# Kernel optimization log

Measured on AMD Instinct MI355X. Metric: run time of the kernel, lower is better.

The kernel has to match this reference:

```python
import jax, jax.numpy as jnp
import numpy as np
from jax import lax

# --- config matching init_kwargs ---
VOXEL_SIZE = np.array([0.25, 0.25, 8.0], np.float32)
PC_RANGE = np.array([-50.0, -50.0, -5.0, 50.0, 50.0, 3.0], np.float32)
MAX_PTS = 32
MAX_VOX = 60000
GRID = np.round((PC_RANGE[3:] - PC_RANGE[:3]) / VOXEL_SIZE).astype(np.int64)  # [400,400,1] (x,y,z)
GX, GY, GZ = int(GRID[0]), int(GRID[1]), int(GRID[2])
BIG = GX * GY * GZ  # sentinel flat id for out-of-range points
N_POINTS = 1_200_000
N_FEATS = 5


def voxelize(points):
    """points: [N, 3+C] float. Returns (out_voxels [V,P,3+C], out_coords [V,3] zyx, out_num_points [V])."""
    N = points.shape[0]
    vsize = jnp.asarray(VOXEL_SIZE)
    vmin = jnp.asarray(PC_RANGE[:3])
    # integer voxel coords per point (x,y,z)
    cxyz = jnp.floor((points[:, :3] - vmin) / vsize).astype(jnp.int32)  # [N,3]
    grid = jnp.asarray(GRID, jnp.int32)
    in_range = jnp.all((cxyz >= 0) & (cxyz < grid), axis=-1)  # [N]
    flat = cxyz[:, 2] * (GY * GX) + cxyz[:, 1] * GX + cxyz[:, 0]
    flat = jnp.where(in_range, flat, BIG)
    # stable sort by voxel id: points within a voxel keep original order (like CPU fill order)
    order = jnp.argsort(flat, stable=True)
    sf = flat[order]                      # sorted flat ids, invalid (BIG) at end
    sp = points[order]                    # [N, D]
    sc = cxyz[order]                      # [N, 3]
    ar = jnp.arange(N, dtype=jnp.int32)
    valid = sf < BIG
    new_seg = jnp.concatenate([jnp.ones((1,), bool), sf[1:] != sf[:-1]])
    first = valid & new_seg               # first point of each non-empty voxel
    vox_idx = jnp.cumsum(first.astype(jnp.int32)) - 1          # voxel slot per point
    seg_start = lax.associative_scan(jnp.maximum, jnp.where(first, ar, 0))
    rank = ar - seg_start                 # position of point within its voxel
    keep = valid & (vox_idx < MAX_VOX) & (rank < MAX_PTS)
    # out-of-bound index MAX_VOX + mode='drop' discards non-kept points
    sv = jnp.where(keep, vox_idx, MAX_VOX)
    sr = jnp.where(keep, rank, 0)
    D = points.shape[1]
    out_voxels = jnp.zeros((MAX_VOX, MAX_PTS, D), points.dtype).at[sv, sr].set(sp, mode='drop')
    out_num_points = jnp.zeros((MAX_VOX,), jnp.int32).at[sv].add(
        keep.astype(jnp.int32), mode='drop')
    coords_zyx = sc[:, ::-1]              # reorder to [z,y,x] as in the torch module
    out_coords = jnp.zeros((MAX_VOX, 3), jnp.int32).at[sv].set(coords_zyx, mode='drop')
    return out_voxels, out_coords, out_num_points


def setup_inputs() -> dict:
    key = jax.random.key(0)
    u = jax.random.uniform(key, (N_POINTS, N_FEATS), jnp.float32)
    # xyz spans slightly beyond the valid range so out-of-range masking is exercised
    lo = jnp.array([-55.0, -55.0, -6.0, 0.0, 0.0], jnp.float32)
    hi = jnp.array([55.0, 55.0, 4.0, 1.0, 1.0], jnp.float32)
    points = lo + u * (hi - lo)
    return {"points": points}


def reference(points):
    return voxelize(points)
```

## Files before the change

### kernel.cpp

```cpp
#include <hip/hip_runtime.h>


constexpr int GXc = 400;
constexpr int GYc = 400;
constexpr int NCELL = GXc * GYc;
constexpr int MAXV  = 60000;
constexpr int MAXP  = 32;
constexpr int NF    = 5;

constexpr int SCAN_B = 256;
constexpr int SCAN_E = 8;
constexpr int SCAN_TILE = SCAN_B * SCAN_E;
constexpr int NSCANBLK = (NCELL + SCAN_TILE - 1) / SCAN_TILE;

__device__ __forceinline__ int point_cell(float x, float y, float z) {
    int cx = (int)floorf((x + 50.0f) * 4.0f);
    int cy = (int)floorf((y + 50.0f) * 4.0f);
    int cz = (int)floorf((z + 5.0f) * 0.125f);
    if (cx < 0 || cx >= GXc || cy < 0 || cy >= GYc || cz != 0) return -1;
    return cy * GXc + cx;
}

__global__ void __launch_bounds__(256)
k_bin(const float* __restrict__ pts, int N,
      unsigned char* __restrict__ occupied, int* __restrict__ cellId) {
    int t = blockIdx.x * blockDim.x + threadIdx.x;
    int i0 = t * 4;
    if (i0 >= N) return;
    if (N - i0 >= 4) {
        const float4* src = (const float4*)(pts + (size_t)i0 * NF);
        float4 q0 = src[0], q1 = src[1], q2 = src[2], q3 = src[3], q4 = src[4];
        float f[20];
        *(float4*)(f + 0)  = q0; *(float4*)(f + 4)  = q1; *(float4*)(f + 8)  = q2;
        *(float4*)(f + 12) = q3; *(float4*)(f + 16) = q4;
        int cs[4];
        #pragma unroll
        for (int k = 0; k < 4; k++)
            cs[k] = point_cell(f[k * 5 + 0], f[k * 5 + 1], f[k * 5 + 2]);
        *(int4*)(cellId + i0) = make_int4(cs[0], cs[1], cs[2], cs[3]);
        #pragma unroll
        for (int k = 0; k < 4; k++)
            if (cs[k] >= 0) occupied[cs[k]] = 1;
    } else {
        for (int k = 0; k < N - i0; k++) {
            const float* p = pts + (size_t)(i0 + k) * NF;
            int c = point_cell(p[0], p[1], p[2]);
            cellId[i0 + k] = c;
            if (c >= 0) occupied[c] = 1;
        }
    }
}

__global__ void k_scanA(const unsigned char* __restrict__ occupied,
                        int* __restrict__ excl, int* __restrict__ blockSums) {
    __shared__ int sh[SCAN_B];
    int base = blockIdx.x * SCAN_TILE;
    int idx0 = base + threadIdx.x * SCAN_E;
    unsigned long long occ8 = 0;
    if (idx0 < NCELL) occ8 = *(const unsigned long long*)(occupied + idx0);
    int vals[SCAN_E];
    int sum = 0;
    #pragma unroll
    for (int e = 0; e < SCAN_E; e++) {
        int v = (int)((occ8 >> (8 * e)) & 1ull);
        vals[e] = sum;
        sum += v;
    }
    sh[threadIdx.x] = sum;
    __syncthreads();
    for (int off = 1; off < SCAN_B; off <<= 1) {
        int t = (threadIdx.x >= (unsigned)off) ? sh[threadIdx.x - off] : 0;
        __syncthreads();
        sh[threadIdx.x] += t;
        __syncthreads();
    }
    int thrExcl = (threadIdx.x == 0) ? 0 : sh[threadIdx.x - 1];
    #pragma unroll
    for (int e = 0; e < SCAN_E; e++) {
        int idx = idx0 + e;
        if (idx < NCELL) excl[idx] = thrExcl + vals[e];
    }
    if (threadIdx.x == SCAN_B - 1) blockSums[blockIdx.x] = sh[SCAN_B - 1];
}

__global__ void k_scanB(const unsigned char* __restrict__ occupied,
                        const int* __restrict__ excl,
                        const int* __restrict__ blockSums,
                        int* __restrict__ voxId,
                        int* __restrict__ cellOfVox,
                        int* __restrict__ nvoxOut) {
    __shared__ int sb[128];
    int tid = threadIdx.x;
    if (tid < 128) sb[tid] = (tid < NSCANBLK) ? blockSums[tid] : 0;
    __syncthreads();
    for (int off = 1; off < 128; off <<= 1) {
        int t = (tid < 128 && tid >= off) ? sb[tid - off] : 0;
        __syncthreads();
        if (tid < 128) sb[tid] += t;
        __syncthreads();
    }
    int c = blockIdx.x * blockDim.x + tid;
    if (c < NCELL) {
        int vi = -1;
        if (occupied[c]) {
            int blk = c / SCAN_TILE;
            int basev = (blk == 0) ? 0 : sb[blk - 1];
            int v = basev + excl[c];
            if (v < MAXV) { vi = v; cellOfVox[v] = c; }
        }
        voxId[c] = vi;
    }
    if (blockIdx.x == 0 && tid == 0) {
        int tot = sb[NSCANBLK - 1];
        *nvoxOut = tot < MAXV ? tot : MAXV;
    }
}

__global__ void __launch_bounds__(256)
k_scatter2(const int* __restrict__ cellId, int N,
           const int* __restrict__ voxId,
           int* __restrict__ vcount, int* __restrict__ slots) {
    int t = blockIdx.x * blockDim.x + threadIdx.x;
    int i0 = t * 8;
    if (i0 >= N) return;
    if (N - i0 >= 8) {
        int4 a = *(const int4*)(cellId + i0);
        int4 b = *(const int4*)(cellId + i0 + 4);
        int cs[8] = {a.x, a.y, a.z, a.w, b.x, b.y, b.z, b.w};
        int vs[8];
        #pragma unroll
        for (int k = 0; k < 8; k++)
            vs[k] = (cs[k] >= 0) ? voxId[cs[k]] : -1;
        #pragma unroll
        for (int k = 0; k < 8; k++) {
            if (vs[k] >= 0) {
                int pos = atomicAdd(&vcount[vs[k]], 1);
                if (pos < MAXP) slots[vs[k] * MAXP + pos] = i0 + k;
            }
        }
    } else {
        for (int k = 0; k < N - i0; k++) {
            int c = cellId[i0 + k];
            if (c >= 0) {
                int v = voxId[c];
                if (v >= 0) {
                    int pos = atomicAdd(&vcount[v], 1);
                    if (pos < MAXP) slots[v * MAXP + pos] = i0 + k;
                }
            }
        }
    }
}

__global__ void __launch_bounds__(256)
k_finalize(const float* __restrict__ pts, int N,
           const int* __restrict__ vcount,
           const int* __restrict__ slots,
           const int* __restrict__ cellOfVox,
           const int* __restrict__ nvoxPtr,
           float* __restrict__ outVox,
           float* __restrict__ outCoord,
           float* __restrict__ outNum) {
    __shared__ int   s_key[4][4][MAXP];
    __shared__ int   s_srt[4][4][MAXP];
    __shared__ float s_dat[4][4][MAXP * NF];

    int tid  = threadIdx.x;
    int wv   = tid >> 6, lane = tid & 63;
    int h    = lane >> 5, s = lane & 31;
    int vb   = (blockIdx.x * 4 + wv) * 4;
    int nvox = *nvoxPtr;

    int u0 = vb + h, u1 = vb + 2 + h;
    bool live0 = u0 < nvox, live1 = u1 < nvox;
    int num0 = 0, num1 = 0;
    if (live0) { int cnt = vcount[u0]; num0 = cnt < MAXP ? cnt : MAXP; }
    if (live1) { int cnt = vcount[u1]; num1 = cnt < MAXP ? cnt : MAXP; }

    int k0 = (live0 && s < num0) ? slots[u0 * MAXP + s] : 0x7fffffff;
    int k1 = (live1 && s < num1) ? slots[u1 * MAXP + s] : 0x7fffffff;
    s_key[wv][h][s]     = k0;
    s_key[wv][2 + h][s] = k1;

    float* flat = (float*)s_dat[wv];
    #pragma unroll
    for (int q = 0; q < 10; q++) flat[q * 64 + lane] = 0.0f;

    int rank0 = 0, rank1 = 0;
    #pragma unroll
    for (int j = 0; j < MAXP; j++) rank0 += (s_key[wv][h][j] < k0) ? 1 : 0;
    #pragma unroll
    for (int j = 0; j < MAXP; j++) rank1 += (s_key[wv][2 + h][j] < k1) ? 1 : 0;
    bool g0 = live0 && s < num0, g1 = live1 && s < num1;
    if (g0) s_srt[wv][h][rank0]     = k0;
    if (g1) s_srt[wv][2 + h][rank1] = k1;

    int p0 = g0 ? s_srt[wv][h][s]     : 0;
    int p1 = g1 ? s_srt[wv][2 + h][s] : 0;
    float4 qa0, qb0, qa1, qb1;
    int sel0 = -1, sel1 = -1;
    size_t lim = (size_t)N * 20;
    const float4* f4 = (const float4*)pts;
    if (g0) {
        size_t b = (size_t)p0 * 20;
        if (b + 32 <= lim) {
            sel0 = (int)((b & 15) >> 2);
            size_t w = b >> 4;
            qa0 = f4[w]; qb0 = f4[w + 1];
        }
    }
    if (g1) {
        size_t b = (size_t)p1 * 20;
        if (b + 32 <= lim) {
            sel1 = (int)((b & 15) >> 2);
            size_t w = b >> 4;
            qa1 = f4[w]; qb1 = f4[w + 1];
        }
    }
    if (g0) {
        float r0, r1, r2, r3, r4, r5, r6, r7;
        if (sel0 >= 0) {
            r0 = qa0.x; r1 = qa0.y; r2 = qa0.z; r3 = qa0.w;
            r4 = qb0.x; r5 = qb0.y; r6 = qb0.z; r7 = qb0.w;
        } else {
            const float* sp = pts + (size_t)p0 * NF;
            r0 = sp[0]; r1 = sp[1]; r2 = sp[2]; r3 = sp[3]; r4 = sp[4];
            r5 = r6 = r7 = 0.0f; sel0 = 0;
        }
        float o0 = sel0 == 0 ? r0 : sel0 == 1 ? r1 : sel0 == 2 ? r2 : r3;
        float o1 = sel0 == 0 ? r1 : sel0 == 1 ? r2 : sel0 == 2 ? r3 : r4;
        float o2 = sel0 == 0 ? r2 : sel0 == 1 ? r3 : sel0 == 2 ? r4 : r5;
        float o3 = sel0 == 0 ? r3 : sel0 == 1 ? r4 : sel0 == 2 ? r5 : r6;
        float o4 = sel0 == 0 ? r4 : sel0 == 1 ? r5 : sel0 == 2 ? r6 : r7;
        float* d = &s_dat[wv][h][s * NF];
        d[0] = o0; d[1] = o1; d[2] = o2; d[3] = o3; d[4] = o4;
    }
    if (g1) {
        float r0, r1, r2, r3, r4, r5, r6, r7;
        if (sel1 >= 0) {
            r0 = qa1.x; r1 = qa1.y; r2 = qa1.z; r3 = qa1.w;
            r4 = qb1.x; r5 = qb1.y; r6 = qb1.z; r7 = qb1.w;
        } else {
            const float* sp = pts + (size_t)p1 * NF;
            r0 = sp[0]; r1 = sp[1]; r2 = sp[2]; r3 = sp[3]; r4 = sp[4];
            r5 = r6 = r7 = 0.0f; sel1 = 0;
        }
        float o0 = sel1 == 0 ? r0 : sel1 == 1 ? r1 : sel1 == 2 ? r2 : r3;
        float o1 = sel1 == 0 ? r1 : sel1 == 1 ? r2 : sel1 == 2 ? r3 : r4;
        float o2 = sel1 == 0 ? r2 : sel1 == 1 ? r3 : sel1 == 2 ? r4 : r5;
        float o3 = sel1 == 0 ? r3 : sel1 == 1 ? r4 : sel1 == 2 ? r5 : r6;
        float o4 = sel1 == 0 ? r4 : sel1 == 1 ? r5 : sel1 == 2 ? r6 : r7;
        float* d = &s_dat[wv][2 + h][s * NF];
        d[0] = o0; d[1] = o1; d[2] = o2; d[3] = o3; d[4] = o4;
    }

    const float4* sv = (const float4*)s_dat[wv];
    float4* dst = (float4*)(outVox + (size_t)vb * (MAXP * NF));
    #pragma unroll
    for (int q = 0; q < 3; q++) {
        int idx = q * 64 + lane;
        if (idx < 160) dst[idx] = sv[idx];
    }
    if (lane < 4) {
        int v = vb + lane;
        bool lv = v < nvox;
        int c = lv ? cellOfVox[v] : 0;
        int cnt = lv ? vcount[v] : 0;
        int num = cnt < MAXP ? cnt : MAXP;
        outNum[v] = lv ? (float)num : 0.0f;
        outCoord[(size_t)v * 3 + 0] = 0.0f;
        outCoord[(size_t)v * 3 + 1] = lv ? (float)(c / GXc) : 0.0f;
        outCoord[(size_t)v * 3 + 2] = lv ? (float)(c % GXc) : 0.0f;
    }
}

extern "C" void kernel_launch(void* const* d_in, const int* in_sizes, int n_in,
                              void* d_out, int out_size, void* d_ws, size_t ws_size,
                              hipStream_t stream) {
    const float* pts = (const float*)d_in[0];
    int N = in_sizes[0] / NF;

    float* out      = (float*)d_out;
    float* outVox   = out;
    float* outCoord = out + (size_t)MAXV * MAXP * NF;
    float* outNum   = outCoord + (size_t)MAXV * 3;

    char* ws = (char*)d_ws;
    auto take = [&](size_t bytes) {
        char* p = ws;
        ws += (bytes + 255) & ~(size_t)255;
        return p;
    };
    unsigned char* occupied = (unsigned char*)take((size_t)NCELL);
    int* vcount    = (int*)take((size_t)MAXV * 4);
    int* cellId    = (int*)take((size_t)((N + 7) & ~7) * 4);
    int* excl      = (int*)take((size_t)NCELL * 4);
    int* blockSums = (int*)take((size_t)128 * 4);
    int* voxId     = (int*)take((size_t)NCELL * 4);
    int* cellOfVox = (int*)take((size_t)MAXV * 4);
    int* slots     = (int*)take((size_t)MAXV * MAXP * 4);
    int* nvoxBuf   = (int*)take(256);

    size_t zeroBytes = (size_t)((char*)(vcount + MAXV) - (char*)occupied);
    hipMemsetAsync(occupied, 0, zeroBytes, stream);

    int nb4 = ((N + 3) / 4 + 255) / 256;
    k_bin<<<nb4, 256, 0, stream>>>(pts, N, occupied, cellId);
    k_scanA<<<NSCANBLK, SCAN_B, 0, stream>>>(occupied, excl, blockSums);
    k_scanB<<<(NCELL + 255) / 256, 256, 0, stream>>>(occupied, excl, blockSums,
                                                     voxId, cellOfVox, nvoxBuf);
    int nb8 = ((N + 7) / 8 + 255) / 256;
    k_scatter2<<<nb8, 256, 0, stream>>>(cellId, N, voxId, vcount, slots);
    k_finalize<<<MAXV / 16, 256, 0, stream>>>(pts, N, vcount, slots, cellOfVox,
                                              nvoxBuf, outVox, outCoord, outNum);
}
```

Before: 120.7 us.

## Scatter full point payloads into voxel slots and drop cellId buffer

```diff
diff --git a/kernel.cpp b/kernel.cpp
--- a/kernel.cpp
+++ b/kernel.cpp
@@ -22,8 +22,104 @@
 }
 
 __global__ void __launch_bounds__(256)
-k_bin(const float* __restrict__ pts, int N,
-      unsigned char* __restrict__ occupied, int* __restrict__ cellId) {
+k_bin(const float* __restrict__ pts, int N, unsigned char* __restrict__ occupied) {
+    int t = blockIdx.x * blockDim.x + threadIdx.x;
+    int i0 = t * 4;
+    if (i0 >= N) return;
+    if (N - i0 >= 4) {
+        const float4* src = (const float4*)(pts + (size_t)i0 * NF);
+        float4 q0 = src[0], q1 = src[1], q2 = src[2], q3 = src[3], q4 = src[4];
+        float f[20];
+        *(float4*)(f + 0)  = q0; *(float4*)(f + 4)  = q1; *(float4*)(f + 8)  = q2;
+        *(float4*)(f + 12) = q3; *(float4*)(f + 16) = q4;
+        #pragma unroll
+        for (int k = 0; k < 4; k++) {
+            int c = point_cell(f[k * 5 + 0], f[k * 5 + 1], f[k * 5 + 2]);
+            if (c >= 0) occupied[c] = 1;
+        }
+    } else {
+        for (int k = 0; k < N - i0; k++) {
+            const float* p = pts + (size_t)(i0 + k) * NF;
+            int c = point_cell(p[0], p[1], p[2]);
+            if (c >= 0) occupied[c] = 1;
+        }
+    }
+}
+
+__global__ void k_scanA(const unsigned char* __restrict__ occupied,
+                        int* __restrict__ excl, int* __restrict__ blockSums) {
+    __shared__ int sh[SCAN_B];
+    int base = blockIdx.x * SCAN_TILE;
+    int idx0 = base + threadIdx.x * SCAN_E;
+    unsigned long long occ8 = 0;
+    if (idx0 < NCELL) occ8 = *(const unsigned long long*)(occupied + idx0);
+    int vals[SCAN_E];
+    int sum = 0;
+    #pragma unroll
+    for (int e = 0; e < SCAN_E; e++) {
+        int v = (int)((occ8 >> (8 * e)) & 1ull);
+        vals[e] = sum;
+        sum += v;
+    }
+    sh[threadIdx.x] = sum;
+    __syncthreads();
+    for (int off = 1; off < SCAN_B; off <<= 1) {
+        int t = (threadIdx.x >= (unsigned)off) ? sh[threadIdx.x - off] : 0;
+        __syncthreads();
+        sh[threadIdx.x] += t;
+        __syncthreads();
+    }
+    int thrExcl = (threadIdx.x == 0) ? 0 : sh[threadIdx.x - 1];
+    #pragma unroll
+    for (int e = 0; e < SCAN_E; e++) {
+        int idx = idx0 + e;
+        if (idx < NCELL) excl[idx] = thrExcl + vals[e];
+    }
+    if (threadIdx.x == SCAN_B - 1) blockSums[blockIdx.x] = sh[SCAN_B - 1];
+}
+
+__global__ void k_scanB(const unsigned char* __restrict__ occupied,
+                        const int* __restrict__ excl,
+                        const int* __restrict__ blockSums,
+                        int* __restrict__ voxId,
+                        int* __restrict__ cellOfVox,
+                        int* __restrict__ vcount,
+                        int* __restrict__ nvoxOut) {
+    __shared__ int sb[128];
+    int tid = threadIdx.x;
+    if (tid < 128) sb[tid] = (tid < NSCANBLK) ? blockSums[tid] : 0;
+    __syncthreads();
+    for (int off = 1; off < 128; off <<= 1) {
+        int t = (tid < 128 && tid >= off) ? sb[tid - off] : 0;
+        __syncthreads();
+        if (tid < 128) sb[tid] += t;
+        __syncthreads();
+    }
+    int c = blockIdx.x * blockDim.x + tid;
+    if (c < NCELL) {
+        int vi = -1;
+        if (occupied[c]) {
+            int blk = c / SCAN_TILE;
+            int basev = (blk == 0) ? 0 : sb[blk - 1];
+            int v = basev + excl[c];
+            if (v < MAXV) {
+                vi = v;
+                cellOfVox[v] = c;
+                vcount[v] = 0;
+            }
+        }
+        voxId[c] = vi;
+    }
+    if (blockIdx.x == 0 && tid == 0) {
+        int tot = sb[NSCANBLK - 1];
+        *nvoxOut = tot < MAXV ? tot : MAXV;
+    }
+}
+
+__global__ void __launch_bounds__(256)
+k_scatter3(const float* __restrict__ pts, int N,
+           const int* __restrict__ voxId,
+           int* __restrict__ vcount, float* __restrict__ vdata) {
     int t = blockIdx.x * blockDim.x + threadIdx.x;
     int i0 = t * 4;
     if (i0 >= N) return;
@@ -37,115 +133,36 @@
         #pragma unroll
         for (int k = 0; k < 4; k++)
             cs[k] = point_cell(f[k * 5 + 0], f[k * 5 + 1], f[k * 5 + 2]);
-        *(int4*)(cellId + i0) = make_int4(cs[0], cs[1], cs[2], cs[3]);
+        int vs[4];
         #pragma unroll
         for (int k = 0; k < 4; k++)
-            if (cs[k] >= 0) occupied[cs[k]] = 1;
+            vs[k] = (cs[k] >= 0) ? voxId[cs[k]] : -1;
+        #pragma unroll
+        for (int k = 0; k < 4; k++) {
+            if (vs[k] >= 0) {
+                int pos = atomicAdd(&vcount[vs[k]], 1);
+                if (pos < MAXP) {
+                    float* r = vdata + ((size_t)vs[k] * MAXP + pos) * 8;
+                    *(float4*)r = make_float4(f[k*5+0], f[k*5+1], f[k*5+2], f[k*5+3]);
+                    *(float4*)(r + 4) = make_float4(f[k*5+4],
+                                                    __int_as_float(i0 + k), 0.0f, 0.0f);
+                }
+            }
+        }
     } else {
         for (int k = 0; k < N - i0; k++) {
             const float* p = pts + (size_t)(i0 + k) * NF;
             int c = point_cell(p[0], p[1], p[2]);
-            cellId[i0 + k] = c;
-            if (c >= 0) occupied[c] = 1;
-        }
-    }
-}
-
-__global__ void k_scanA(const unsigned char* __restrict__ occupied,
-                        int* __restrict__ excl, int* __restrict__ blockSums) {
-    __shared__ int sh[SCAN_B];
-    int base = blockIdx.x * SCAN_TILE;
-    int idx0 = base + threadIdx.x * SCAN_E;
-    unsigned long long occ8 = 0;
-    if (idx0 < NCELL) occ8 = *(const unsigned long long*)(occupied + idx0);
-    int vals[SCAN_E];
-    int sum = 0;
-    #pragma unroll
-    for (int e = 0; e < SCAN_E; e++) {
-        int v = (int)((occ8 >> (8 * e)) & 1ull);
-        vals[e] = sum;
-        sum += v;
-    }
-    sh[threadIdx.x] = sum;
-    __syncthreads();
-    for (int off = 1; off < SCAN_B; off <<= 1) {
-        int t = (threadIdx.x >= (unsigned)off) ? sh[threadIdx.x - off] : 0;
-        __syncthreads();
-        sh[threadIdx.x] += t;
-        __syncthreads();
-    }
-    int thrExcl = (threadIdx.x == 0) ? 0 : sh[threadIdx.x - 1];
-    #pragma unroll
-    for (int e = 0; e < SCAN_E; e++) {
-        int idx = idx0 + e;
-        if (idx < NCELL) excl[idx] = thrExcl + vals[e];
-    }
-    if (threadIdx.x == SCAN_B - 1) blockSums[blockIdx.x] = sh[SCAN_B - 1];
-}
-
-__global__ void k_scanB(const unsigned char* __restrict__ occupied,
-                        const int* __restrict__ excl,
-                        const int* __restrict__ blockSums,
-                        int* __restrict__ voxId,
-                        int* __restrict__ cellOfVox,
-                        int* __restrict__ nvoxOut) {
-    __shared__ int sb[128];
-    int tid = threadIdx.x;
-    if (tid < 128) sb[tid] = (tid < NSCANBLK) ? blockSums[tid] : 0;
-    __syncthreads();
-    for (int off = 1; off < 128; off <<= 1) {
-        int t = (tid < 128 && tid >= off) ? sb[tid - off] : 0;
-        __syncthreads();
-        if (tid < 128) sb[tid] += t;
-        __syncthreads();
-    }
-    int c = blockIdx.x * blockDim.x + tid;
-    if (c < NCELL) {
-        int vi = -1;
-        if (occupied[c]) {
-            int blk = c / SCAN_TILE;
-            int basev = (blk == 0) ? 0 : sb[blk - 1];
-            int v = basev + excl[c];
-            if (v < MAXV) { vi = v; cellOfVox[v] = c; }
-        }
-        voxId[c] = vi;
-    }
-    if (blockIdx.x == 0 && tid == 0) {
-        int tot = sb[NSCANBLK - 1];
-        *nvoxOut = tot < MAXV ? tot : MAXV;
-    }
-}
-
-__global__ void __launch_bounds__(256)
-k_scatter2(const int* __restrict__ cellId, int N,
-           const int* __restrict__ voxId,
-           int* __restrict__ vcount, int* __restrict__ slots) {
-    int t = blockIdx.x * blockDim.x + threadIdx.x;
-    int i0 = t * 8;
-    if (i0 >= N) return;
-    if (N - i0 >= 8) {
-        int4 a = *(const int4*)(cellId + i0);
-        int4 b = *(const int4*)(cellId + i0 + 4);
-        int cs[8] = {a.x, a.y, a.z, a.w, b.x, b.y, b.z, b.w};
-        int vs[8];
-        #pragma unroll
-        for (int k = 0; k < 8; k++)
-            vs[k] = (cs[k] >= 0) ? voxId[cs[k]] : -1;
-        #pragma unroll
-        for (int k = 0; k < 8; k++) {
-            if (vs[k] >= 0) {
-                int pos = atomicAdd(&vcount[vs[k]], 1);
-                if (pos < MAXP) slots[vs[k] * MAXP + pos] = i0 + k;
-            }
-        }
-    } else {
-        for (int k = 0; k < N - i0; k++) {
-            int c = cellId[i0 + k];
             if (c >= 0) {
                 int v = voxId[c];
                 if (v >= 0) {
                     int pos = atomicAdd(&vcount[v], 1);
-                    if (pos < MAXP) slots[v * MAXP + pos] = i0 + k;
+                    if (pos < MAXP) {
+                        float* r = vdata + ((size_t)v * MAXP + pos) * 8;
+                        *(float4*)r = make_float4(p[0], p[1], p[2], p[3]);
+                        *(float4*)(r + 4) = make_float4(p[4],
+                                                        __int_as_float(i0 + k), 0.0f, 0.0f);
+                    }
                 }
             }
         }
@@ -153,16 +170,14 @@
 }
 
 __global__ void __launch_bounds__(256)
-k_finalize(const float* __restrict__ pts, int N,
-           const int* __restrict__ vcount,
-           const int* __restrict__ slots,
-           const int* __restrict__ cellOfVox,
-           const int* __restrict__ nvoxPtr,
-           float* __restrict__ outVox,
-           float* __restrict__ outCoord,
-           float* __restrict__ outNum) {
+k_finalize2(const int* __restrict__ vcount,
+            const float* __restrict__ vdata,
+            const int* __restrict__ cellOfVox,
+            const int* __restrict__ nvoxPtr,
+            float* __restrict__ outVox,
+            float* __restrict__ outCoord,
+            float* __restrict__ outNum) {
     __shared__ int   s_key[4][4][MAXP];
-    __shared__ int   s_srt[4][4][MAXP];
     __shared__ float s_dat[4][4][MAXP * NF];
 
     int tid  = threadIdx.x;
@@ -176,9 +191,19 @@
     int num0 = 0, num1 = 0;
     if (live0) { int cnt = vcount[u0]; num0 = cnt < MAXP ? cnt : MAXP; }
     if (live1) { int cnt = vcount[u1]; num1 = cnt < MAXP ? cnt : MAXP; }
-
-    int k0 = (live0 && s < num0) ? slots[u0 * MAXP + s] : 0x7fffffff;
-    int k1 = (live1 && s < num1) ? slots[u1 * MAXP + s] : 0x7fffffff;
+    bool g0 = live0 && s < num0, g1 = live1 && s < num1;
+
+    float4 a0, b0, a1, b1;
+    if (g0) {
+        const float4* r = (const float4*)(vdata + ((size_t)u0 * MAXP + s) * 8);
+        a0 = r[0]; b0 = r[1];
+    }
+    if (g1) {
+        const float4* r = (const float4*)(vdata + ((size_t)u1 * MAXP + s) * 8);
+        a1 = r[0]; b1 = r[1];
+    }
+    int k0 = g0 ? __float_as_int(b0.y) : 0x7fffffff;
+    int k1 = g1 ? __float_as_int(b1.y) : 0x7fffffff;
     s_key[wv][h][s]     = k0;
     s_key[wv][2 + h][s] = k1;
 
@@ -191,67 +216,13 @@
     for (int j = 0; j < MAXP; j++) rank0 += (s_key[wv][h][j] < k0) ? 1 : 0;
     #pragma unroll
     for (int j = 0; j < MAXP; j++) rank1 += (s_key[wv][2 + h][j] < k1) ? 1 : 0;
-    bool g0 = live0 && s < num0, g1 = live1 && s < num1;
-    if (g0) s_srt[wv][h][rank0]     = k0;
-    if (g1) s_srt[wv][2 + h][rank1] = k1;
-
-    int p0 = g0 ? s_srt[wv][h][s]     : 0;
-    int p1 = g1 ? s_srt[wv][2 + h][s] : 0;
-    float4 qa0, qb0, qa1, qb1;
-    int sel0 = -1, sel1 = -1;
-    size_t lim = (size_t)N * 20;
-    const float4* f4 = (const float4*)pts;
     if (g0) {
-        size_t b = (size_t)p0 * 20;
-        if (b + 32 <= lim) {
-            sel0 = (int)((b & 15) >> 2);
-            size_t w = b >> 4;
-            qa0 = f4[w]; qb0 = f4[w + 1];
-        }
+        float* d = &s_dat[wv][h][rank0 * NF];
+        d[0] = a0.x; d[1] = a0.y; d[2] = a0.z; d[3] = a0.w; d[4] = b0.x;
     }
     if (g1) {
-        size_t b = (size_t)p1 * 20;
-        if (b + 32 <= lim) {
-            sel1 = (int)((b & 15) >> 2);
-            size_t w = b >> 4;
-            qa1 = f4[w]; qb1 = f4[w + 1];
-        }
-    }
-    if (g0) {
-        float r0, r1, r2, r3, r4, r5, r6, r7;
-        if (sel0 >= 0) {
-            r0 = qa0.x; r1 = qa0.y; r2 = qa0.z; r3 = qa0.w;
-            r4 = qb0.x; r5 = qb0.y; r6 = qb0.z; r7 = qb0.w;
-        } else {
-            const float* sp = pts + (size_t)p0 * NF;
-            r0 = sp[0]; r1 = sp[1]; r2 = sp[2]; r3 = sp[3]; r4 = sp[4];
-            r5 = r6 = r7 = 0.0f; sel0 = 0;
-        }
-        float o0 = sel0 == 0 ? r0 : sel0 == 1 ? r1 : sel0 == 2 ? r2 : r3;
-        float o1 = sel0 == 0 ? r1 : sel0 == 1 ? r2 : sel0 == 2 ? r3 : r4;
-        float o2 = sel0 == 0 ? r2 : sel0 == 1 ? r3 : sel0 == 2 ? r4 : r5;
-        float o3 = sel0 == 0 ? r3 : sel0 == 1 ? r4 : sel0 == 2 ? r5 : r6;
-        float o4 = sel0 == 0 ? r4 : sel0 == 1 ? r5 : sel0 == 2 ? r6 : r7;
-        float* d = &s_dat[wv][h][s * NF];
-        d[0] = o0; d[1] = o1; d[2] = o2; d[3] = o3; d[4] = o4;
-    }
-    if (g1) {
-        float r0, r1, r2, r3, r4, r5, r6, r7;
-        if (sel1 >= 0) {
-            r0 = qa1.x; r1 = qa1.y; r2 = qa1.z; r3 = qa1.w;
-            r4 = qb1.x; r5 = qb1.y; r6 = qb1.z; r7 = qb1.w;
-        } else {
-            const float* sp = pts + (size_t)p1 * NF;
-            r0 = sp[0]; r1 = sp[1]; r2 = sp[2]; r3 = sp[3]; r4 = sp[4];
-            r5 = r6 = r7 = 0.0f; sel1 = 0;
-        }
-        float o0 = sel1 == 0 ? r0 : sel1 == 1 ? r1 : sel1 == 2 ? r2 : r3;
-        float o1 = sel1 == 0 ? r1 : sel1 == 1 ? r2 : sel1 == 2 ? r3 : r4;
-        float o2 = sel1 == 0 ? r2 : sel1 == 1 ? r3 : sel1 == 2 ? r4 : r5;
-        float o3 = sel1 == 0 ? r3 : sel1 == 1 ? r4 : sel1 == 2 ? r5 : r6;
-        float o4 = sel1 == 0 ? r4 : sel1 == 1 ? r5 : sel1 == 2 ? r6 : r7;
-        float* d = &s_dat[wv][2 + h][s * NF];
-        d[0] = o0; d[1] = o1; d[2] = o2; d[3] = o3; d[4] = o4;
+        float* d = &s_dat[wv][2 + h][rank1 * NF];
+        d[0] = a1.x; d[1] = a1.y; d[2] = a1.z; d[3] = a1.w; d[4] = b1.x;
     }
 
     const float4* sv = (const float4*)s_dat[wv];
@@ -293,24 +264,21 @@
     };
     unsigned char* occupied = (unsigned char*)take((size_t)NCELL);
     int* vcount    = (int*)take((size_t)MAXV * 4);
-    int* cellId    = (int*)take((size_t)((N + 7) & ~7) * 4);
     int* excl      = (int*)take((size_t)NCELL * 4);
     int* blockSums = (int*)take((size_t)128 * 4);
     int* voxId     = (int*)take((size_t)NCELL * 4);
     int* cellOfVox = (int*)take((size_t)MAXV * 4);
-    int* slots     = (int*)take((size_t)MAXV * MAXP * 4);
+    float* vdata   = (float*)take((size_t)MAXV * MAXP * 8 * 4);
     int* nvoxBuf   = (int*)take(256);
 
-    size_t zeroBytes = (size_t)((char*)(vcount + MAXV) - (char*)occupied);
-    hipMemsetAsync(occupied, 0, zeroBytes, stream);
+    hipMemsetAsync(occupied, 0, (size_t)NCELL, stream);
 
     int nb4 = ((N + 3) / 4 + 255) / 256;
-    k_bin<<<nb4, 256, 0, stream>>>(pts, N, occupied, cellId);
+    k_bin<<<nb4, 256, 0, stream>>>(pts, N, occupied);
     k_scanA<<<NSCANBLK, SCAN_B, 0, stream>>>(occupied, excl, blockSums);
     k_scanB<<<(NCELL + 255) / 256, 256, 0, stream>>>(occupied, excl, blockSums,
-                                                     voxId, cellOfVox, nvoxBuf);
-    int nb8 = ((N + 7) / 8 + 255) / 256;
-    k_scatter2<<<nb8, 256, 0, stream>>>(cellId, N, voxId, vcount, slots);
-    k_finalize<<<MAXV / 16, 256, 0, stream>>>(pts, N, vcount, slots, cellOfVox,
-                                              nvoxBuf, outVox, outCoord, outNum);
-}
+                                                     voxId, cellOfVox, vcount, nvoxBuf);
+    k_scatter3<<<nb4, 256, 0, stream>>>(pts, N, voxId, vcount, vdata);
+    k_finalize2<<<MAXV / 16, 256, 0, stream>>>(vcount, vdata, cellOfVox,
+                                               nvoxBuf, outVox, outCoord, outNum);
+}
```

After: 114.1 us. 1.06x faster.
